# Performance work log

Hardware: AMD Instinct MI355X
Metric: run time of the kernel (lower is better)

## Reference

```python
import jax, jax.numpy as jnp
import numpy as np

C = 256      # in_channels
CI = 128     # inter_channels = in_channels // 2
B, H, W = 16, 64, 64
EPS = 1e-5   # BatchNorm2d default eps


def conv1x1(x, w, b=None):
    # x: (b,c,h,w), w: (o,c) -> (b,o,h,w)
    out = jnp.einsum('bchw,oc->bohw', x, w)
    if b is not None:
        out = out + b[None, :, None, None]
    return out


def maxpool2x2(x):
    b, c, h, w = x.shape
    return x.reshape(b, c, h // 2, 2, w // 2, 2).max(axis=(3, 5))


def setup_inputs() -> dict:
    key = jax.random.key(0)
    ks = jax.random.split(key, 12)
    s_in = 1.0 / np.sqrt(C)
    s_int = 1.0 / np.sqrt(CI)
    return {
        'x': jax.random.normal(ks[0], (B, C, H, W), jnp.float32),
        'y': jax.random.normal(ks[1], (B, C, H, W), jnp.float32),
        'theta_w': jax.random.uniform(ks[2], (CI, C), jnp.float32, -s_in, s_in),
        'theta_b': jax.random.uniform(ks[3], (CI,), jnp.float32, -s_in, s_in),
        'phi_w': jax.random.uniform(ks[4], (CI, C), jnp.float32, -s_in, s_in),
        'phi_b': jax.random.uniform(ks[5], (CI,), jnp.float32, -s_in, s_in),
        'g_w': jax.random.uniform(ks[6], (CI, C), jnp.float32, -s_in, s_in),
        'g_b': jax.random.uniform(ks[7], (CI,), jnp.float32, -s_in, s_in),
        'W_w': jax.random.uniform(ks[8], (C, CI), jnp.float32, -s_int, s_int),
        'W_b': jax.random.uniform(ks[9], (C,), jnp.float32, -s_int, s_int),
        'bn_gamma': jax.random.normal(ks[10], (C,), jnp.float32) * 0.1,
        'bn_beta': jax.random.normal(ks[11], (C,), jnp.float32) * 0.1,
    }


def reference(x, y, theta_w, theta_b, phi_w, phi_b, g_w, g_b, W_w, W_b, bn_gamma, bn_beta):
    b, c, h, w = x.shape
    # g branch: 1x1 conv on y + 2x2 maxpool -> (b, CI, hw/4) -> (b, hw/4, CI)
    g_y = maxpool2x2(conv1x1(y, g_w, g_b)).reshape(b, CI, -1).transpose(0, 2, 1)
    # theta branch: 1x1 conv on x -> (b, hw, CI)
    theta_x = conv1x1(x, theta_w, theta_b).reshape(b, CI, -1).transpose(0, 2, 1)
    # phi branch: 1x1 conv on y + maxpool -> (b, CI, hw/4)
    phi_y = maxpool2x2(conv1x1(y, phi_w, phi_b)).reshape(b, CI, -1)
    # attention: (b, hw, hw/4)
    f = jnp.einsum('bnc,bcm->bnm', theta_x, phi_y)
    f_div_C = jax.nn.softmax(f, axis=-1)
    # z: (b, hw, CI) -> (b, CI, h, w)
    z = jnp.einsum('bnm,bmc->bnc', f_div_C, g_y)
    z = z.transpose(0, 2, 1).reshape(b, CI, h, w)
    # W: 1x1 conv + BatchNorm2d (training-mode batch stats, biased var)
    wz = conv1x1(z, W_w, W_b)
    mean = wz.mean(axis=(0, 2, 3), keepdims=True)
    var = wz.var(axis=(0, 2, 3), keepdims=True)
    wz = (wz - mean) * jax.lax.rsqrt(var + EPS)
    wz = wz * bn_gamma[None, :, None, None] + bn_beta[None, :, None, None]
    return wz + x
```

## Files before the change

kernel.cpp:

```cpp
#include <hip/hip_runtime.h>
#include <cstdint>

#define HW 4096
#define NC 256
#define CI 128
#define NB 16
#define MP 1024

typedef __bf16 bfv8 __attribute__((ext_vector_type(8)));
typedef float f32x16 __attribute__((ext_vector_type(16)));

__device__ __forceinline__ uint32_t bfr(float x) {
    uint32_t u = __float_as_uint(x);
    return (u + 0x7fffu + ((u >> 16) & 1u)) >> 16;
}
__device__ __forceinline__ uint32_t pkbf(float a, float b) {
    return bfr(a) | (bfr(b) << 16);
}
__device__ __forceinline__ float b2f_lo(uint32_t u) { return __uint_as_float(u << 16); }
__device__ __forceinline__ float b2f_hi(uint32_t u) { return __uint_as_float(u & 0xffff0000u); }

__global__ void k_castw(const float* __restrict__ a, const float* __restrict__ b,
                        const float* __restrict__ c, const float* __restrict__ d,
                        ushort* __restrict__ dst) {
    const float* srcs[4] = {a, b, c, d};
    const float* s = srcs[blockIdx.y];
    int i = (blockIdx.x * 256 + threadIdx.x) * 8;
    float4 v0 = *(const float4*)(s + i);
    float4 v1 = *(const float4*)(s + i + 4);
    uint4 o;
    o.x = pkbf(v0.x, v0.y); o.y = pkbf(v0.z, v0.w);
    o.z = pkbf(v1.x, v1.y); o.w = pkbf(v1.z, v1.w);
    *(uint4*)(dst + (size_t)blockIdx.y * 32768 + i) = o;
}

template<int O_TILE, int NT>
__global__ __launch_bounds__(256) void k_conv_mfma(
        const float* __restrict__ in, const ushort* __restrict__ wbf,
        const float* __restrict__ bias0, const float* __restrict__ bias1,
        ushort* __restrict__ outT) {
    __shared__ ushort xs[NT * 256];
    const int t = threadIdx.x;
    constexpr int tilesPerB = 4096 / NT;
    const int b = blockIdx.x / tilesPerB;
    const int n0 = (blockIdx.x % tilesPerB) * NT;
    const float* inb = in + ((size_t)b * 256) * 4096 + n0;

    constexpr int RPP = 1024 / NT;
    const int c0 = t % RPP, q = t / RPP;
    #pragma unroll
    for (int p = 0; p < 256 / RPP; p++) {
        int c = c0 + p * RPP;
        float4 v = *(const float4*)(inb + (size_t)c * 4096 + q * 4);
        #pragma unroll
        for (int j = 0; j < 4; j++) {
            int n = q * 4 + j;
            xs[n * 256 + (c ^ ((n & 7) << 3))] = (ushort)bfr((&v.x)[j]);
        }
    }
    __syncthreads();

    const int lane = t & 63, w = t >> 6;
    const int ln = lane & 31, hi = lane >> 5;
    int ob0, nb0;
    if (O_TILE == 256) { ob0 = w * 2; nb0 = 0; }
    else               { ob0 = (w & 1) * 2; nb0 = (w >> 1) * 2; }

    f32x16 acc[2][2];
    #pragma unroll
    for (int i = 0; i < 2; i++)
        #pragma unroll
        for (int j = 0; j < 2; j++)
            #pragma unroll
            for (int k = 0; k < 16; k++) acc[i][j][k] = 0.f;

    const ushort* wr0 = wbf + (size_t)(ob0 * 32 + ln) * 256 + hi * 8;
    const ushort* wr1 = wr0 + 32 * 256;
    const int nr0 = nb0 * 32 + ln, nr1 = nr0 + 32;
    const int sw0 = (nr0 & 7) << 3, sw1 = (nr1 & 7) << 3;

    #pragma unroll 4
    for (int ks = 0; ks < 16; ks++) {
        int k = ks * 16 + hi * 8;
        bfv8 wf0 = *(const bfv8*)(wr0 + ks * 16);
        bfv8 wf1 = *(const bfv8*)(wr1 + ks * 16);
        bfv8 x0 = *(const bfv8*)&xs[nr0 * 256 + (k ^ sw0)];
        bfv8 x1 = *(const bfv8*)&xs[nr1 * 256 + (k ^ sw1)];
        acc[0][0] = __builtin_amdgcn_mfma_f32_32x32x16_bf16(wf0, x0, acc[0][0], 0, 0, 0);
        acc[0][1] = __builtin_amdgcn_mfma_f32_32x32x16_bf16(wf0, x1, acc[0][1], 0, 0, 0);
        acc[1][0] = __builtin_amdgcn_mfma_f32_32x32x16_bf16(wf1, x0, acc[1][0], 0, 0, 0);
        acc[1][1] = __builtin_amdgcn_mfma_f32_32x32x16_bf16(wf1, x1, acc[1][1], 0, 0, 0);
    }

    #pragma unroll
    for (int oi = 0; oi < 2; oi++) {
        int obb = (ob0 + oi) * 32;
        #pragma unroll
        for (int grp = 0; grp < 4; grp++) {
            int og = obb + grp * 8 + hi * 4;
            const float* bp = (O_TILE == 256 && og >= 128) ? bias1 : bias0;
            float4 bv = *(const float4*)&bp[og & 127];
            #pragma unroll
            for (int ni = 0; ni < 2; ni++) {
                int n = n0 + (nb0 + ni) * 32 + ln;
                float r0 = acc[oi][ni][grp * 4 + 0] + bv.x;
                float r1 = acc[oi][ni][grp * 4 + 1] + bv.y;
                float r2 = acc[oi][ni][grp * 4 + 2] + bv.z;
                float r3 = acc[oi][ni][grp * 4 + 3] + bv.w;
                uint2 pk;
                pk.x = pkbf(r0, r1); pk.y = pkbf(r2, r3);
                *(uint2*)&outT[((size_t)b * 4096 + n) * O_TILE + og] = pk;
            }
        }
    }
}

__global__ __launch_bounds__(512) void k_convpool(
        const float* __restrict__ in, const ushort* __restrict__ wbf,
        const float* __restrict__ bias0, const float* __restrict__ bias1,
        ushort* __restrict__ phiT, ushort* __restrict__ gout) {
    __shared__ char lds[65536];
    ushort* xs = (ushort*)lds;
    const int t = threadIdx.x;
    const int b = blockIdx.x >> 5;
    const int r = blockIdx.x & 31;
    const int n0 = r * 128;
    const float* inb = in + ((size_t)b * 256) * 4096 + n0;

    {
        const int c0 = t & 7, qq = t >> 3;
        const int ch = qq >> 5, n4 = (qq & 31) * 4;
        #pragma unroll
        for (int p = 0; p < 16; p++) {
            int c = c0 + ch * 8 + p * 16;
            float4 v = *(const float4*)(inb + (size_t)c * 4096 + n4);
            #pragma unroll
            for (int j = 0; j < 4; j++) {
                int n = n4 + j;
                xs[n * 256 + (c ^ ((n & 7) << 3))] = (ushort)bfr((&v.x)[j]);
            }
        }
    }
    __syncthreads();

    const int lane = t & 63, w = t >> 6;
    const int ln = lane & 31, hi = lane >> 5;
    const int ob0 = (w & 3) * 2;
    const int nb0 = (w >> 2) * 2;
    const int lr = nb0 >> 1;

    f32x16 acc[2][2];
    #pragma unroll
    for (int i = 0; i < 2; i++)
        #pragma unroll
        for (int j = 0; j < 2; j++)
            #pragma unroll
            for (int k = 0; k < 16; k++) acc[i][j][k] = 0.f;

    const ushort* wr0 = wbf + (size_t)(ob0 * 32 + ln) * 256 + hi * 8;
    const ushort* wr1 = wr0 + 32 * 256;
    const int nr0 = nb0 * 32 + ln, nr1 = nr0 + 32;
    const int sw0 = (nr0 & 7) << 3, sw1 = (nr1 & 7) << 3;

    #pragma unroll 4
    for (int ks = 0; ks < 16; ks++) {
        int k = ks * 16 + hi * 8;
        bfv8 wf0 = *(const bfv8*)(wr0 + ks * 16);
        bfv8 wf1 = *(const bfv8*)(wr1 + ks * 16);
        bfv8 x0 = *(const bfv8*)&xs[nr0 * 256 + (k ^ sw0)];
        bfv8 x1 = *(const bfv8*)&xs[nr1 * 256 + (k ^ sw1)];
        acc[0][0] = __builtin_amdgcn_mfma_f32_32x32x16_bf16(wf0, x0, acc[0][0], 0, 0, 0);
        acc[0][1] = __builtin_amdgcn_mfma_f32_32x32x16_bf16(wf0, x1, acc[0][1], 0, 0, 0);
        acc[1][0] = __builtin_amdgcn_mfma_f32_32x32x16_bf16(wf1, x0, acc[1][0], 0, 0, 0);
        acc[1][1] = __builtin_amdgcn_mfma_f32_32x32x16_bf16(wf1, x1, acc[1][1], 0, 0, 0);
    }

    __syncthreads();
    float* poolreg = (float*)lds + lr * 8192;

    #pragma unroll
    for (int oi = 0; oi < 2; oi++) {
        #pragma unroll
        for (int grp = 0; grp < 4; grp++) {
            int og = (ob0 + oi) * 32 + grp * 8 + hi * 4;
            const float* bp = (og >= 128) ? bias1 : bias0;
            float4 bv = *(const float4*)&bp[og & 127];
            #pragma unroll
            for (int ni = 0; ni < 2; ni++) {
                #pragma unroll
                for (int j = 0; j < 4; j++) {
                    float v = acc[oi][ni][grp * 4 + j] + (&bv.x)[j];
                    float hm = fmaxf(v, __shfl_xor(v, 1, 64));
                    if ((ln & 1) == 0) {
                        int o = og + j;
                        poolreg[(o << 5) + ni * 16 + (ln >> 1)] = hm;
                    }
                }
            }
        }
    }
    __syncthreads();

    const float* p0 = (const float*)lds;
    const float* p1 = (const float*)lds + 8192;
    {
        int m = t >> 4, ci8 = (t & 15) * 8;
        uint32_t pk4[4];
        #pragma unroll
        for (int jp = 0; jp < 4; jp++) {
            int o0 = ci8 + jp * 2;
            float f0 = fmaxf(p0[(o0 << 5) + m], p1[(o0 << 5) + m]);
            float f1 = fmaxf(p0[((o0 + 1) << 5) + m], p1[((o0 + 1) << 5) + m]);
            pk4[jp] = pkbf(f0, f1);
        }
        *(uint4*)&phiT[((size_t)b * MP + r * 32 + m) * CI + ci8] =
            make_uint4(pk4[0], pk4[1], pk4[2], pk4[3]);
    }
    {
        int ci = t >> 2, mq = (t & 3) * 8;
        int o = 128 + ci;
        uint32_t pk4[4];
        #pragma unroll
        for (int jp = 0; jp < 4; jp++) {
            int mm = mq + jp * 2;
            float f0 = fmaxf(p0[(o << 5) + mm], p1[(o << 5) + mm]);
            float f1 = fmaxf(p0[(o << 5) + mm + 1], p1[(o << 5) + mm + 1]);
            pk4[jp] = pkbf(f0, f1);
        }
        *(uint4*)&gout[((size_t)b * CI + ci) * MP + r * 32 + mq] =
            make_uint4(pk4[0], pk4[1], pk4[2], pk4[3]);
    }
}

__global__ __launch_bounds__(512, 2) void k_attn_mfma(
        const ushort* __restrict__ thetaT, const ushort* __restrict__ phiT,
        const ushort* __restrict__ gmat, ushort* __restrict__ zout) {
    __shared__ char lds[65536];
    const int t = threadIdx.x;
    const int w = t >> 6, lane = t & 63;
    const int nq = lane & 31, hi = lane >> 5;
    const int b = blockIdx.x >> 4;
    const int q0 = (blockIdx.x & 15) << 8;

    {
        int row = t >> 1, s0 = (t & 1) * 8;
        const uint4* src = (const uint4*)(thetaT + ((size_t)b * HW + q0 + row) * CI) + s0;
        uint4* dstrow = (uint4*)(lds + row * 256);
        int rsw = row & 15;
        #pragma unroll
        for (int j = 0; j < 8; j++) {
            uint4 v = src[j];
            dstrow[(s0 + j) ^ rsw] = v;
        }
    }
    __syncthreads();
    bfv8 qf[8];
    {
        int row = w * 32 + nq;
        int rsw = nq & 15;
        #pragma unroll
        for (int ks = 0; ks < 8; ks++) {
            qf[ks] = *(const bfv8*)(lds + row * 256 + (((ks * 2 + hi) ^ rsw) << 4));
        }
    }
    __syncthreads();

    f32x16 zacc[4];
    #pragma unroll
    for (int ct = 0; ct < 4; ct++)
        #pragma unroll
        for (int i = 0; i < 16; i++) zacc[ct][i] = 0.f;
    float run_sum = 0.f;

    const int kind = t >> 8;
    const int tt = t & 255;
    const int prow = tt >> 2, ps0 = (tt & 3) * 4;
    const int grow_i = tt >> 1, gs0 = (tt & 1) * 4;

    const int rswp = nq & 15;
    const int rswg = nq & 7;

    auto issue_loads = [&](int it, uint4* pf) {
        if (kind == 0) {
            const uint4* src = (const uint4*)(phiT + ((size_t)b * MP + it * 64 + prow) * CI) + ps0;
            #pragma unroll
            for (int j = 0; j < 4; j++) pf[j] = src[j];
        } else {
            const uint4* src = (const uint4*)(gmat + ((size_t)b * CI + grow_i) * MP + it * 64) + gs0;
            #pragma unroll
            for (int j = 0; j < 4; j++) pf[j] = src[j];
        }
    };
    auto write_tile = [&](int buf, const uint4* pf) {
        if (kind == 0) {
            uint4* dstrow = (uint4*)(lds + buf * 32768 + prow * 256);
            int rsw = prow & 15;
            #pragma unroll
            for (int j = 0; j < 4; j++) dstrow[(ps0 + j) ^ rsw] = pf[j];
        } else {
            uint4* dstrow = (uint4*)(lds + buf * 32768 + 16384 + grow_i * 128);
            int rsw = grow_i & 7;
            #pragma unroll
            for (int j = 0; j < 4; j++) dstrow[(gs0 + j) ^ rsw] = pf[j];
        }
    };

    {
        uint4 pf[4];
        issue_loads(0, pf);
        write_tile(0, pf);
    }
    __syncthreads();

    for (int it = 0; it < 16; it++) {
        uint4 pf[4];
        if (it < 15) issue_loads(it + 1, pf);

        const char* phiB = lds + (it & 1) * 32768;
        const char* gB   = phiB + 16384;

        f32x16 sA, sB;
        #pragma unroll
        for (int i = 0; i < 16; i++) { sA[i] = 0.f; sB[i] = 0.f; }
        __builtin_amdgcn_s_setprio(1);
        #pragma unroll
        for (int ks = 0; ks < 8; ks++) {
            int slot = ks * 2 + hi;
            bfv8 a0 = *(const bfv8*)(phiB + nq * 256 + ((slot ^ rswp) << 4));
            bfv8 a1 = *(const bfv8*)(phiB + (32 + nq) * 256 + ((slot ^ rswp) << 4));
            sA = __builtin_amdgcn_mfma_f32_32x32x16_bf16(a0, qf[ks], sA, 0, 0, 0);
            sB = __builtin_amdgcn_mfma_f32_32x32x16_bf16(a1, qf[ks], sB, 0, 0, 0);
        }
        __builtin_amdgcn_s_setprio(0);

        float pA[16], pB[16];
        #pragma unroll
        for (int i = 0; i < 16; i++) { pA[i] = __expf(sA[i]); run_sum += pA[i]; }
        #pragma unroll
        for (int i = 0; i < 16; i++) { pB[i] = __expf(sB[i]); run_sum += pB[i]; }

        uint32_t wA[8], wB[8], tA[8], tB[8];
        #pragma unroll
        for (int j = 0; j < 8; j++) { wA[j] = pkbf(pA[2 * j], pA[2 * j + 1]); wB[j] = pkbf(pB[2 * j], pB[2 * j + 1]); }
        #pragma unroll
        for (int j = 0; j < 8; j++) { tA[j] = (uint32_t)__shfl_xor((int)wA[j], 32, 64); tB[j] = (uint32_t)__shfl_xor((int)wB[j], 32, 64); }
        bool lo = (hi == 0);
        union PU { uint32_t u[4]; bfv8 v; } p0A, p1A, p0B, p1B;
        p0A.u[0] = lo ? wA[0] : tA[2]; p0A.u[1] = lo ? wA[1] : tA[3];
        p0A.u[2] = lo ? tA[0] : wA[2]; p0A.u[3] = lo ? tA[1] : wA[3];
        p1A.u[0] = lo ? wA[4] : tA[6]; p1A.u[1] = lo ? wA[5] : tA[7];
        p1A.u[2] = lo ? tA[4] : wA[6]; p1A.u[3] = lo ? tA[5] : wA[7];
        p0B.u[0] = lo ? wB[0] : tB[2]; p0B.u[1] = lo ? wB[1] : tB[3];
        p0B.u[2] = lo ? tB[0] : wB[2]; p0B.u[3] = lo ? tB[1] : wB[3];
        p1B.u[0] = lo ? wB[4] : tB[6]; p1B.u[1] = lo ? wB[5] : tB[7];
        p1B.u[2] = lo ? tB[4] : wB[6]; p1B.u[3] = lo ? tB[5] : wB[7];

        __builtin_amdgcn_s_setprio(1);
        #pragma unroll
        for (int ct = 0; ct < 4; ct++) {
            const char* grw = gB + (ct * 32 + nq) * 128;
            bfv8 g0 = *(const bfv8*)(grw + (((0 * 2 + hi) ^ rswg) << 4));
            bfv8 g1 = *(const bfv8*)(grw + (((1 * 2 + hi) ^ rswg) << 4));
            bfv8 g2 = *(const bfv8*)(grw + (((2 * 2 + hi) ^ rswg) << 4));
            bfv8 g3 = *(const bfv8*)(grw + (((3 * 2 + hi) ^ rswg) << 4));
            zacc[ct] = __builtin_amdgcn_mfma_f32_32x32x16_bf16(g0, p0A.v, zacc[ct], 0, 0, 0);
            zacc[ct] = __builtin_amdgcn_mfma_f32_32x32x16_bf16(g1, p1A.v, zacc[ct], 0, 0, 0);
            zacc[ct] = __builtin_amdgcn_mfma_f32_32x32x16_bf16(g2, p0B.v, zacc[ct], 0, 0, 0);
            zacc[ct] = __builtin_amdgcn_mfma_f32_32x32x16_bf16(g3, p1B.v, zacc[ct], 0, 0, 0);
        }
        __builtin_amdgcn_s_setprio(0);

        if (it < 15) write_tile((it + 1) & 1, pf);
        __syncthreads();
    }

    float pair_sum = run_sum + __shfl_xor(run_sum, 32, 64);
    float rinv = 1.f / pair_sum;
    ushort* zr = zout + ((size_t)b * HW + q0 + w * 32 + nq) * CI;
    #pragma unroll
    for (int ct = 0; ct < 4; ct++) {
        #pragma unroll
        for (int grp = 0; grp < 4; grp++) {
            int c0 = ct * 32 + grp * 8 + hi * 4;
            uint2 pk;
            pk.x = pkbf(zacc[ct][grp * 4 + 0] * rinv, zacc[ct][grp * 4 + 1] * rinv);
            pk.y = pkbf(zacc[ct][grp * 4 + 2] * rinv, zacc[ct][grp * 4 + 3] * rinv);
            *(uint2*)(zr + c0) = pk;
        }
    }
}

__global__ __launch_bounds__(256) void k_wz_mfma(
        const ushort* __restrict__ z, const ushort* __restrict__ Wbf,
        const float* __restrict__ Wb, ushort* __restrict__ wz,
        float* __restrict__ part) {
    __shared__ ushort zs[128 * 128];
    int t = threadIdx.x;
    int mtile = blockIdx.x;
    int oh = blockIdx.y;
    int b = mtile >> 5;
    int n0 = (mtile & 31) << 7;
    const ushort* zt = z + ((size_t)b * 4096 + n0) * 128;
    #pragma unroll
    for (int it = 0; it < 8; it++) {
        int d = (it * 256 + t) * 16;
        uint4 v = *(const uint4*)((const char*)zt + d);
        int n = d >> 8;
        int widx = (n << 7) + (((d & 255) ^ ((n & 7) << 4)) >> 1);
        *(uint4*)&zs[widx] = v;
    }
    __syncthreads();
    int lane = t & 63, w = t >> 6;
    int ln = lane & 31, hi = lane >> 5;
    int wr = w >> 1, wc = w & 1;
    f32x16 acc[2][2];
    #pragma unroll
    for (int i = 0; i < 2; i++)
        #pragma unroll
        for (int j = 0; j < 2; j++)
            #pragma unroll
            for (int k = 0; k < 16; k++) acc[i][j][k] = 0.f;
    const ushort* w0 = Wbf + (size_t)(oh * 128 + wc * 64 + ln) * 128 + hi * 8;
    const ushort* w1 = w0 + 32 * 128;
    int nr0 = wr * 64 + ln, nr1 = nr0 + 32;
    int sw0 = (nr0 & 7) << 3, sw1 = (nr1 & 7) << 3;
    #pragma unroll
    for (int ks = 0; ks < 8; ks++) {
        int k = ks * 16 + hi * 8;
        bfv8 a0 = *(const bfv8*)&zs[(nr0 << 7) + (k ^ sw0)];
        bfv8 a1 = *(const bfv8*)&zs[(nr1 << 7) + (k ^ sw1)];
        bfv8 b0 = *(const bfv8*)(w0 + ks * 16);
        bfv8 b1 = *(const bfv8*)(w1 + ks * 16);
        acc[0][0] = __builtin_amdgcn_mfma_f32_32x32x16_bf16(a0, b0, acc[0][0], 0, 0, 0);
        acc[0][1] = __builtin_amdgcn_mfma_f32_32x32x16_bf16(a0, b1, acc[0][1], 0, 0, 0);
        acc[1][0] = __builtin_amdgcn_mfma_f32_32x32x16_bf16(a1, b0, acc[1][0], 0, 0, 0);
        acc[1][1] = __builtin_amdgcn_mfma_f32_32x32x16_bf16(a1, b1, acc[1][1], 0, 0, 0);
    }
    #pragma unroll
    for (int obi = 0; obi < 2; obi++) {
        int o = oh * 128 + wc * 64 + obi * 32 + ln;
        float bv = Wb[o];
        ushort* orow = wz + ((size_t)b * 256 + o) * 4096 + n0;
        float s = 0.f, qq = 0.f;
        #pragma unroll
        for (int nbi = 0; nbi < 2; nbi++) {
            #pragma unroll
            for (int grp = 0; grp < 4; grp++) {
                float vals[4];
                #pragma unroll
                for (int j = 0; j < 4; j++) {
                    float v = acc[nbi][obi][grp * 4 + j] + bv;
                    vals[j] = v;
                    s += v; qq += v * v;
                }
                int n = (wr * 2 + nbi) * 32 + grp * 8 + hi * 4;
                uint2 pk;
                pk.x = pkbf(vals[0], vals[1]);
                pk.y = pkbf(vals[2], vals[3]);
                *(uint2*)(orow + n) = pk;
            }
        }
        s += __shfl_xor(s, 32, 64);
        qq += __shfl_xor(qq, 32, 64);
        if (hi == 0) {
            float* pr = part + (size_t)(mtile * 2 + wr) * 512;
            pr[o] = s;
            pr[256 + o] = qq;
        }
    }
}

__global__ __launch_bounds__(256) void k_bnstats(const float* __restrict__ part,
        const float* __restrict__ gamma, const float* __restrict__ beta,
        float* __restrict__ ss) {
    int o = blockIdx.x, t = threadIdx.x;
    float s = 0.f, q = 0.f;
    for (int k = t; k < 1024; k += 256) {
        s += part[(size_t)k * 512 + o];
        q += part[(size_t)k * 512 + 256 + o];
    }
    #pragma unroll
    for (int d = 32; d > 0; d >>= 1) { s += __shfl_down(s, d, 64); q += __shfl_down(q, d, 64); }
    __shared__ float rs[4], rq[4];
    int wave = t >> 6, lane = t & 63;
    if (lane == 0) { rs[wave] = s; rq[wave] = q; }
    __syncthreads();
    if (t == 0) {
        float S = rs[0] + rs[1] + rs[2] + rs[3];
        float Q = rq[0] + rq[1] + rq[2] + rq[3];
        const float inv = 1.0f / 65536.0f;
        float mean = S * inv;
        float var = Q * inv - mean * mean;
        float sc = gamma[o] * rsqrtf(var + 1e-5f);
        ss[o] = sc;
        ss[NC + o] = beta[o] - mean * sc;
    }
}

__global__ void k_apply(float* __restrict__ out, const ushort* __restrict__ wz,
        const float* __restrict__ x, const float* __restrict__ ss) {
    size_t i = ((size_t)blockIdx.x * 256 + threadIdx.x) * 8;
    int o = (int)((i >> 12) & 255);
    float sc = ss[o], sh = ss[NC + o];
    uint4 wv = *(const uint4*)(wz + i);
    float4 x0 = *(const float4*)(x + i);
    float4 x1 = *(const float4*)(x + i + 4);
    float4 r0, r1;
    r0.x = b2f_lo(wv.x) * sc + sh + x0.x;
    r0.y = b2f_hi(wv.x) * sc + sh + x0.y;
    r0.z = b2f_lo(wv.y) * sc + sh + x0.z;
    r0.w = b2f_hi(wv.y) * sc + sh + x0.w;
    r1.x = b2f_lo(wv.z) * sc + sh + x1.x;
    r1.y = b2f_hi(wv.z) * sc + sh + x1.y;
    r1.z = b2f_lo(wv.w) * sc + sh + x1.z;
    r1.w = b2f_hi(wv.w) * sc + sh + x1.w;
    *(float4*)(out + i) = r0;
    *(float4*)(out + i + 4) = r1;
}

extern "C" void kernel_launch(void* const* d_in, const int* in_sizes, int n_in,
                              void* d_out, int out_size, void* d_ws, size_t ws_size,
                              hipStream_t stream) {
    const float* x       = (const float*)d_in[0];
    const float* y       = (const float*)d_in[1];
    const float* theta_w = (const float*)d_in[2];
    const float* theta_b = (const float*)d_in[3];
    const float* phi_w   = (const float*)d_in[4];
    const float* phi_b   = (const float*)d_in[5];
    const float* g_w     = (const float*)d_in[6];
    const float* g_b     = (const float*)d_in[7];
    const float* W_w     = (const float*)d_in[8];
    const float* W_b     = (const float*)d_in[9];
    const float* bn_g    = (const float*)d_in[10];
    const float* bn_b    = (const float*)d_in[11];
    float* ws  = (float*)d_ws;
    float* out = (float*)d_out;

    ushort* wbf    = (ushort*)ws;
    ushort* thetaT = (ushort*)(ws + 65536);
    ushort* wzbf   = (ushort*)(ws + 65536);
    ushort* zbuf   = (ushort*)(ws + 8454144);
    ushort* phiT   = (ushort*)(ws + 12648448);
    ushort* gbuf   = (ushort*)(ws + 13697024);
    float*  part   = ws + 14745600;
    float*  ss     = ws + 15269888;

    k_castw<<<dim3(16, 4), 256, 0, stream>>>(theta_w, phi_w, g_w, W_w, wbf);

    k_conv_mfma<128, 128><<<NB * 32, 256, 0, stream>>>(x, wbf, theta_b, theta_b, thetaT);
    k_convpool<<<NB * 32, 512, 0, stream>>>(y, wbf + 32768, phi_b, g_b, phiT, gbuf);

    k_attn_mfma<<<NB * 16, 512, 0, stream>>>(thetaT, phiT, gbuf, zbuf);

    k_wz_mfma<<<dim3(NB * 32, 2), 256, 0, stream>>>(zbuf, wbf + 98304, W_b, wzbf, part);
    k_bnstats<<<256, 256, 0, stream>>>(part, bn_g, bn_b, ss);
    k_apply<<<8192, 256, 0, stream>>>(out, wzbf, x, ss);
}
```

Measured before the change: 180.9 us.

## Fuse W conv, BatchNorm stats and apply into one cooperative kernel

Replaces the three-kernel tail (W 1x1 conv writing bf16, stats reduction, apply) with one cooperative-launch kernel. It keeps the conv accumulators in registers, writes per-tile partial sums, does a grid-wide sync, has every block reduce all partials itself, and writes normalized output plus residual directly. This removes the intermediate wz round trip through memory and two launches. In exchange, the 512-block grid must be co-resident, each block redundantly reads the full partials buffer, and the grid barrier adds cost. If the cooperative launch fails, the code falls back to the old kernels.

After: 234.9 us. 29.9% more time.

```diff
diff --git a/kernel.cpp b/kernel.cpp
--- a/kernel.cpp
+++ b/kernel.cpp
@@ -1,5 +1,8 @@
 #include <hip/hip_runtime.h>
+#include <hip/hip_cooperative_groups.h>
 #include <cstdint>
+
+namespace cg = cooperative_groups;
 
 #define HW 4096
 #define NC 256
@@ -386,6 +389,122 @@
             pk.x = pkbf(zacc[ct][grp * 4 + 0] * rinv, zacc[ct][grp * 4 + 1] * rinv);
             pk.y = pkbf(zacc[ct][grp * 4 + 2] * rinv, zacc[ct][grp * 4 + 3] * rinv);
             *(uint2*)(zr + c0) = pk;
+        }
+    }
+}
+
+__global__ __launch_bounds__(256, 2) void k_wz_fused(
+        const ushort* __restrict__ z, const ushort* __restrict__ Wbf,
+        const float* __restrict__ Wb, const float* __restrict__ bn_g,
+        const float* __restrict__ bn_b, const float* __restrict__ x,
+        float* __restrict__ out, float* __restrict__ part) {
+    __shared__ ushort zs[128 * 128];
+    const int t = threadIdx.x;
+    const int mtile = blockIdx.x;
+    const int b = mtile >> 5;
+    const int n0 = (mtile & 31) << 7;
+    const ushort* zt = z + ((size_t)b * 4096 + n0) * 128;
+    #pragma unroll
+    for (int it = 0; it < 8; it++) {
+        int d = (it * 256 + t) * 16;
+        uint4 v = *(const uint4*)((const char*)zt + d);
+        int n = d >> 8;
+        int widx = (n << 7) + (((d & 255) ^ ((n & 7) << 4)) >> 1);
+        *(uint4*)&zs[widx] = v;
+    }
+    __syncthreads();
+
+    const int lane = t & 63, w = t >> 6;
+    const int ln = lane & 31, hi = lane >> 5;
+    const int o0 = w * 64;
+
+    f32x16 acc[4][2];
+    #pragma unroll
+    for (int i = 0; i < 4; i++)
+        #pragma unroll
+        for (int j = 0; j < 2; j++)
+            #pragma unroll
+            for (int k = 0; k < 16; k++) acc[i][j][k] = 0.f;
+
+    const ushort* wA = Wbf + (size_t)(o0 + ln) * 128 + hi * 8;
+    const ushort* wB = wA + 32 * 128;
+    int nr[4], sw[4];
+    #pragma unroll
+    for (int nbi = 0; nbi < 4; nbi++) { nr[nbi] = nbi * 32 + ln; sw[nbi] = (nr[nbi] & 7) << 3; }
+
+    #pragma unroll
+    for (int ks = 0; ks < 8; ks++) {
+        int k = ks * 16 + hi * 8;
+        bfv8 b0 = *(const bfv8*)(wA + ks * 16);
+        bfv8 b1 = *(const bfv8*)(wB + ks * 16);
+        #pragma unroll
+        for (int nbi = 0; nbi < 4; nbi++) {
+            bfv8 av = *(const bfv8*)&zs[(nr[nbi] << 7) + (k ^ sw[nbi])];
+            acc[nbi][0] = __builtin_amdgcn_mfma_f32_32x32x16_bf16(av, b0, acc[nbi][0], 0, 0, 0);
+            acc[nbi][1] = __builtin_amdgcn_mfma_f32_32x32x16_bf16(av, b1, acc[nbi][1], 0, 0, 0);
+        }
+    }
+
+    #pragma unroll
+    for (int obi = 0; obi < 2; obi++) {
+        int o = o0 + obi * 32 + ln;
+        float bv = Wb[o];
+        float s = 0.f, qq = 0.f;
+        #pragma unroll
+        for (int nbi = 0; nbi < 4; nbi++) {
+            #pragma unroll
+            for (int k = 0; k < 16; k++) {
+                float v = acc[nbi][obi][k] + bv;
+                acc[nbi][obi][k] = v;
+                s += v; qq += v * v;
+            }
+        }
+        s += __shfl_xor(s, 32, 64);
+        qq += __shfl_xor(qq, 32, 64);
+        if (hi == 0) {
+            float* pr = part + (size_t)mtile * 512;
+            pr[o] = s;
+            pr[256 + o] = qq;
+        }
+    }
+
+    cg::this_grid().sync();
+
+    float S = 0.f, Q = 0.f;
+    {
+        const float* pb = part + o0 + lane;
+        #pragma unroll 8
+        for (int kk = 0; kk < 512; kk++) {
+            S += pb[(size_t)kk * 512];
+            Q += pb[(size_t)kk * 512 + 256];
+        }
+    }
+    const float inv = 1.0f / 65536.0f;
+    float mean = S * inv;
+    float var = Q * inv - mean * mean;
+    float sc_l = bn_g[o0 + lane] * rsqrtf(var + 1e-5f);
+    float sh_l = bn_b[o0 + lane] - mean * sc_l;
+
+    #pragma unroll
+    for (int obi = 0; obi < 2; obi++) {
+        int o = o0 + obi * 32 + ln;
+        float scv = __shfl(sc_l, obi * 32 + ln, 64);
+        float shv = __shfl(sh_l, obi * 32 + ln, 64);
+        float* orow = out + ((size_t)b * 256 + o) * 4096 + n0;
+        const float* xrow = x + ((size_t)b * 256 + o) * 4096 + n0;
+        #pragma unroll
+        for (int nbi = 0; nbi < 4; nbi++) {
+            #pragma unroll
+            for (int grp = 0; grp < 4; grp++) {
+                int n = nbi * 32 + grp * 8 + hi * 4;
+                float4 xv = *(const float4*)(xrow + n);
+                float4 vv;
+                #pragma unroll
+                for (int j = 0; j < 4; j++) {
+                    (&vv.x)[j] = acc[nbi][obi][grp * 4 + j] * scv + shv + (&xv.x)[j];
+                }
+                *(float4*)(orow + n) = vv;
+            }
         }
     }
 }
@@ -552,7 +671,21 @@
 
     k_attn_mfma<<<NB * 16, 512, 0, stream>>>(thetaT, phiT, gbuf, zbuf);
 
-    k_wz_mfma<<<dim3(NB * 32, 2), 256, 0, stream>>>(zbuf, wbf + 98304, W_b, wzbf, part);
-    k_bnstats<<<256, 256, 0, stream>>>(part, bn_g, bn_b, ss);
-    k_apply<<<8192, 256, 0, stream>>>(out, wzbf, x, ss);
-}
+    hipError_t ce;
+    {
+        const ushort* zarg = zbuf;
+        const ushort* warg = wbf + 98304;
+        void* args[] = {
+            (void*)&zarg, (void*)&warg, (void*)&W_b, (void*)&bn_g, (void*)&bn_b,
+            (void*)&x, (void*)&out, (void*)&part
+        };
+        ce = hipLaunchCooperativeKernel((const void*)k_wz_fused,
+                                        dim3(NB * 32), dim3(256), args, 0, stream);
+    }
+    if (ce != hipSuccess) {
+        (void)hipGetLastError();
+        k_wz_mfma<<<dim3(NB * 32, 2), 256, 0, stream>>>(zbuf, wbf + 98304, W_b, wzbf, part);
+        k_bnstats<<<256, 256, 0, stream>>>(part, bn_g, bn_b, ss);
+        k_apply<<<8192, 256, 0, stream>>>(out, wzbf, x, ss);
+    }
+}
```
